# Kernel tuning notes

Measured on AMD Instinct MI355X. Metric: run time of the kernel, lower is better.

Reference implementation:

```python
import jax, jax.numpy as jnp
import numpy as np

B, K, N, D, H, DD, NB, SEQ = 1, 512, 16384, 512, 64, 64, 10, 2048
COREF_PROP = 1  # config['coref_prop']
BIG = 1e23      # additive mask penalty from the torch code


def bucket_distance(d):
    # Lee et al. style log buckets: 0,1,2,3,4, [5-7], [8-15], [16-31], [32-63], [64+]
    d = jnp.abs(d)
    logb = jnp.floor(jnp.log2(jnp.maximum(d, 1).astype(jnp.float32))).astype(d.dtype) + 3
    return jnp.clip(jnp.where(d < 5, d, logb), 0, NB - 1)


def setup_inputs() -> dict:
    key = jax.random.key(0)
    ks = jax.random.split(key, 20)
    rng = np.random.default_rng(0)
    s = 0.02
    span_begin = jnp.sort(jax.random.randint(ks[2], (B, K), 0, SEQ), axis=-1)
    return dict(
        all_span_vecs=jax.random.normal(ks[0], (B, N, D), jnp.float32),
        span_vecs=jax.random.normal(ks[1], (B, K, D), jnp.float32),
        span_begin=span_begin,
        span_end=span_begin + jax.random.randint(ks[3], (B, K), 1, 10),
        triangular_mask=jnp.broadcast_to(jnp.tril(jnp.ones((K, K), jnp.float32), -1), (B, K, K)),
        span_scores=jax.random.normal(ks[4], (B, K, 1), jnp.float32),
        prune_indices=jnp.asarray(np.sort(np.stack([rng.choice(N, K, replace=False) for _ in range(B)]), axis=-1), jnp.int32),
        span_lengths=jnp.full((B,), K, jnp.int32),
        sequence_lengths=jnp.full((B,), SEQ, jnp.int32),
        Wl=jax.random.normal(ks[5], (D, H)) * s, bl=jnp.zeros((H,), jnp.float32),
        Wr=jax.random.normal(ks[6], (D, H)) * s, br=jnp.zeros((H,), jnp.float32),
        Wp=jax.random.normal(ks[7], (D, H)) * s,
        dist_emb=jax.random.normal(ks[8], (NB, DD)) * s,
        Wd=jax.random.normal(ks[9], (DD, H)) * s, bd=jnp.zeros((H,), jnp.float32),
        Wo=jax.random.normal(ks[10], (H, 1)) * s, bo=jnp.zeros((1,), jnp.float32),
        Wg1=jax.random.normal(ks[11], (2 * D, D)) * s, bg1=jnp.zeros((D,), jnp.float32),
        Wg2=jax.random.normal(ks[12], (2 * D, D)) * s, bg2=jnp.zeros((D,), jnp.float32),
        Wpr=jax.random.normal(ks[13], (D, 1)) * s, bpr=jnp.zeros((1,), jnp.float32),
    )


def reference(all_span_vecs, span_vecs, span_begin, span_end, triangular_mask,
              span_scores, prune_indices, span_lengths, sequence_lengths,
              Wl, bl, Wr, br, Wp, dist_emb, Wd, bd, Wo, bo,
              Wg1, bg1, Wg2, bg2, Wpr, bpr):
    # ----- OptFFpairs pairwise scorer: relu(left_i + right_j + prod(v_i*v_j) + dist_ij) -> scalar
    dist_idx = bucket_distance(span_begin[:, :, None] - span_begin[:, None, :])  # [B,K,K]
    dist_feat = dist_emb[dist_idx] @ Wd + bd                                     # [B,K,K,H]

    def pair_scores(u):
        left = u @ Wl + bl                                  # [B,K,H]
        right = u @ Wr + br                                 # [B,K,H]
        prod = jnp.einsum('bid,bjd,dh->bijh', u, u, Wp)     # avoids [B,K,K,D] intermediate
        h = jax.nn.relu(left[:, :, None, :] + right[:, None, :, :] + prod + dist_feat)
        return (h @ Wo + bo)[..., 0]                        # [B,K,K], i.e. squeeze(-1)

    eye = jnp.eye(K, dtype=span_vecs.dtype)[None]

    def add_scores(cs, ss):  # coref_add_scores: add span scores as rows+cols, zero diagonal
        cs = cs + ss + jnp.swapaxes(ss, -1, -2)
        return cs * (1.0 - eye)

    def gate(Wg, bg, left, right):  # MyGate: g = sigmoid(W[l;r]); g*l + (1-g)*r
        g = jax.nn.sigmoid(jnp.concatenate([left, right], -1) @ Wg + bg)
        return g * left + (1.0 - g) * right

    update = span_vecs
    cs = add_scores(pair_scores(update), span_scores)
    m1 = (1.0 - triangular_mask) * BIG
    m2 = (1.0 - jnp.swapaxes(triangular_mask, 1, 2)) * BIG
    for _ in range(COREF_PROP):
        p1 = jax.nn.softmax(cs - m1, axis=-1)
        p2 = jax.nn.softmax(cs - m2, axis=-1)
        c1 = p1 @ update
        c2 = p2 @ update
        update = gate(Wg1, bg1, update, c1) + gate(Wg2, bg2, update, c2)
        # update_coref_scores=True: rescore with pruner(update)
        cs = add_scores(pair_scores(update), update @ Wpr + bpr)

    # ----- overwrite_spans: masked scatter of updated filtered spans into all spans
    mask = (jnp.arange(K)[None, :] < span_lengths[:, None])[..., None]  # [B,K,1]
    b_idx = jnp.arange(B)[:, None]
    orig = all_span_vecs[b_idx, prune_indices]                          # [B,K,D]
    all_out = all_span_vecs.at[b_idx, prune_indices].set(jnp.where(mask, update, orig))
    return all_out, update, cs
```

## Files before the change

### kernel.cpp

```cpp
#include <hip/hip_runtime.h>
#include <hip/hip_bf16.h>


typedef __bf16 bf16;
typedef bf16 bf16x8 __attribute__((ext_vector_type(8)));
typedef float f32x4 __attribute__((ext_vector_type(4)));
typedef float f32x16 __attribute__((ext_vector_type(16)));

#define MFMA16(a, b, c) __builtin_amdgcn_mfma_f32_16x16x32_bf16((a), (b), (c), 0, 0, 0)
#define MFMA32(a, b, c) __builtin_amdgcn_mfma_f32_32x32x16_bf16((a), (b), (c), 0, 0, 0)

__device__ __forceinline__ void gll16(const bf16* g, bf16* lds) {
  __builtin_amdgcn_global_load_lds(
      (const __attribute__((address_space(1))) unsigned int*)g,
      (__attribute__((address_space(3))) unsigned int*)lds, 16, 0, 0);
}

__global__ void k_prep(const float* __restrict__ sv,
                       const float* __restrict__ Wl, const float* __restrict__ Wr,
                       const float* __restrict__ Wg1, const float* __restrict__ Wg2,
                       const float* __restrict__ de, const float* __restrict__ Wd,
                       const float* __restrict__ bd, const float* __restrict__ bl,
                       const float* __restrict__ br, const float* __restrict__ bg1,
                       const float* __restrict__ bg2, const float* __restrict__ Wp,
                       bf16* __restrict__ u1, bf16* __restrict__ ugb,
                       bf16* __restrict__ wlr, float* __restrict__ blbr,
                       float* __restrict__ bgc, bf16* __restrict__ wgb,
                       float* __restrict__ dtab, bf16* __restrict__ wpTb)
{
  const int total = 262144 + 65536 + 128 + 1048576 + 1024 + 640 + 32768;
  for (int idx0 = blockIdx.x * 256 + threadIdx.x; idx0 < total; idx0 += 2048 * 256) {
    int k = idx0;
    if (k < 262144) {
      float v = sv[k]; bf16 b = (bf16)v; u1[k] = b;
      int i = k >> 9, d = k & 511;
      ugb[(long)i * 1024 + d] = b;
      ugb[524288 + (long)i * 1024 + d] = b;
      continue;
    }
    k -= 262144;
    if (k < 65536) {
      int d = k >> 7, h = k & 127;
      wlr[k] = (bf16)(h < 64 ? Wl[d * 64 + h] : Wr[d * 64 + h - 64]);
      continue;
    }
    k -= 65536;
    if (k < 128) { blbr[k] = (k < 64 ? bl[k] : br[k - 64]); continue; }
    k -= 128;
    if (k < 1048576) {
      wgb[k] = (bf16)(k < 524288 ? Wg1[k] : Wg2[k - 524288]);
      continue;
    }
    k -= 1048576;
    if (k < 1024) { bgc[k] = (k < 512 ? bg1[k] : bg2[k - 512]); continue; }
    k -= 1024;
    if (k < 640) {
      int b_ = k >> 6, h = k & 63;
      float s = bd[h];
      for (int e = 0; e < 64; ++e) s += de[b_ * 64 + e] * Wd[e * 64 + h];
      dtab[k] = s;
      continue;
    }
    k -= 640;
    {
      int h = k >> 9, d = k & 511;
      wpTb[k] = (bf16)Wp[d * 64 + h];
    }
  }
}

__global__ __launch_bounds__(256, 2) void k_gemm(
    const bf16* __restrict__ A, int lda, long asz,
    const bf16* __restrict__ B, int ldb, long bsz,
    float* __restrict__ C, int ldc, long csz,
    const float* __restrict__ bias, int bstride, int K,
    bf16* __restrict__ xout)
{
  __shared__ bf16 As[64 * 40];
  __shared__ bf16 Bs[64 * 40];
  const int t = threadIdx.x, lane = t & 63, wave = t >> 6;
  const int tc = blockIdx.x, tr = blockIdx.y, z = blockIdx.z;
  A += (long)z * asz; B += (long)z * bsz; C += (long)z * csz;
  const int wr = wave >> 1, wc = wave & 1;
  const int arow = t >> 2, aslot = t & 3;
  const int s = lane >> 4, rr = lane & 15;
  f32x4 acc00 = {}, acc01 = {}, acc10 = {}, acc11 = {};
  const int nk = K >> 5;
  for (int kk = 0; kk < nk; ++kk) {
    __syncthreads();
    *(uint4*)&As[arow * 40 + aslot * 8] =
        *(const uint4*)(A + (long)(tr * 64 + arow) * lda + kk * 32 + aslot * 8);
    {
      const bf16* bsrc = B + (long)(kk * 32 + aslot * 8) * ldb + tc * 64 + arow;
      bf16x8 tv;
#pragma unroll
      for (int e = 0; e < 8; ++e) tv[e] = bsrc[(long)e * ldb];
      *(bf16x8*)&Bs[arow * 40 + aslot * 8] = tv;
    }
    __syncthreads();
    bf16x8 a0 = *(const bf16x8*)&As[(wr * 32 + rr) * 40 + s * 8];
    bf16x8 a1 = *(const bf16x8*)&As[(wr * 32 + 16 + rr) * 40 + s * 8];
    bf16x8 b0 = *(const bf16x8*)&Bs[(wc * 32 + rr) * 40 + s * 8];
    bf16x8 b1 = *(const bf16x8*)&Bs[(wc * 32 + 16 + rr) * 40 + s * 8];
    acc00 = MFMA16(a0, b0, acc00);
    acc01 = MFMA16(a0, b1, acc01);
    acc10 = MFMA16(a1, b0, acc10);
    acc11 = MFMA16(a1, b1, acc11);
  }
#pragma unroll
  for (int mf = 0; mf < 2; ++mf) {
#pragma unroll
    for (int nf = 0; nf < 2; ++nf) {
      f32x4 v = mf == 0 ? (nf == 0 ? acc00 : acc01) : (nf == 0 ? acc10 : acc11);
      int col = tc * 64 + wc * 32 + nf * 16 + rr;
      float bi = bias ? bias[z * bstride + col] : 0.f;
      int row0 = tr * 64 + wr * 32 + mf * 16 + s * 4;
#pragma unroll
      for (int r = 0; r < 4; ++r) {
        float val = v[r] + bi;
        int row = row0 + r;
        C[(long)row * ldc + col] = val;
        if (xout) {
          long gidx = (row < 512)
              ? ((long)row * 1024 + 512 + col)
              : (524288 + (long)(row - 512) * 1024 + 512 + col);
          xout[gidx] = (bf16)val;
        }
      }
    }
  }
}

__global__ __launch_bounds__(512, 1) void k_pair64(
    const bf16* __restrict__ Ubf, const float* __restrict__ Uf,
    const bf16* __restrict__ wpTb, const float* __restrict__ LR,
    const float* __restrict__ dtabg, const int* __restrict__ sb,
    const float* __restrict__ ss, const float* __restrict__ Wo,
    const float* __restrict__ bo, float* __restrict__ cs,
    const float* __restrict__ copysrc, float* __restrict__ copydst, int docopy)
{
  __shared__ bf16 Apan[2][256 * 64];
  __shared__ bf16 Bpan[2][256 * 64];
  __shared__ float dtsp[10 * 68];
  __shared__ int sbt[256];

  const int t = threadIdx.x;
  const int l = t & 63;
  const int w = t >> 6;
  const int wm = w >> 1, wn = w & 1;
  const int hi = l >> 5, l31 = l & 31;
  const int jb = blockIdx.x;
  const int mt = blockIdx.y;
  const int i0 = mt * 4;
  const int i = i0 + wm;

  for (int idx = t; idx < 640; idx += 512)
    dtsp[(idx >> 6) * 68 + (idx & 63)] = dtabg[idx];
  if (t < 256) sbt[t] = sb[jb * 256 + t];

  const bf16* bsrcq[4];
  bf16* bdstq[4];
#pragma unroll
  for (int q = 0; q < 4; ++q) {
    int u = q * 512 + t;
    int r = u >> 3, c = u & 7;
    bsrcq[q] = Ubf + (long)(jb * 256 + r) * 512 + ((c ^ (r & 7)) * 8);
    bdstq[q] = &Bpan[0][0] + q * 4096 + w * 512;
  }
  const float* uapq[4];
  const bf16* wppq[4];
  int awbq[4];
#pragma unroll
  for (int q = 0; q < 4; ++q) {
    int u = q * 512 + t;
    int m = u >> 3, c = u & 7;
    int koff = (c ^ (m & 7)) * 8;
    uapq[q] = Uf + (long)(i0 + (m >> 6)) * 512 + koff;
    wppq[q] = wpTb + (long)(m & 63) * 512 + koff;
    awbq[q] = m * 128 + c * 16;
  }

  int aoff[2][4], boff[4][4];
#pragma unroll
  for (int rf = 0; rf < 2; ++rf)
#pragma unroll
    for (int ks = 0; ks < 4; ++ks) {
      int r = wm * 64 + rf * 32 + l31;
      aoff[rf][ks] = r * 128 + (((ks * 2 + hi) ^ (r & 7)) * 16);
    }
#pragma unroll
  for (int cf = 0; cf < 4; ++cf)
#pragma unroll
    for (int ks = 0; ks < 4; ++ks) {
      int r = wn * 128 + cf * 32 + l31;
      boff[cf][ks] = r * 128 + (((ks * 2 + hi) ^ (r & 7)) * 16);
    }

  {
#pragma unroll
    for (int q = 0; q < 4; ++q) gll16(bsrcq[q], bdstq[q]);
#pragma unroll
    for (int q = 0; q < 4; ++q) {
      float4 f0 = *(const float4*)uapq[q];
      float4 f1 = *(const float4*)(uapq[q] + 4);
      bf16x8 wv = *(const bf16x8*)wppq[q];
      bf16x8 v;
#pragma unroll
      for (int e = 0; e < 4; ++e) {
        v[e] = (bf16)(f0[e] * (float)wv[e]);
        v[e + 4] = (bf16)(f1[e] * (float)wv[e + 4]);
      }
      *(bf16x8*)((char*)&Apan[0][0] + awbq[q]) = v;
    }
  }
  asm volatile("s_waitcnt vmcnt(0)");
  __syncthreads();

  f32x16 acc[2][4] = {};

  for (int kc = 0; kc < 8; ++kc) {
    const int cur = kc & 1;
    float4 nf0[4], nf1[4];
    bf16x8 nwv[4];
    if (kc < 7) {
#pragma unroll
      for (int q = 0; q < 4; ++q)
        gll16(bsrcq[q] + (kc + 1) * 64, bdstq[q] + (cur ^ 1) * 16384);
#pragma unroll
      for (int q = 0; q < 4; ++q) {
        nf0[q] = *(const float4*)(uapq[q] + (kc + 1) * 64);
        nf1[q] = *(const float4*)(uapq[q] + (kc + 1) * 64 + 4);
        nwv[q] = *(const bf16x8*)(wppq[q] + (kc + 1) * 64);
      }
    }
    const char* Ab = (const char*)&Apan[cur][0];
    const char* Bb = (const char*)&Bpan[cur][0];
#pragma unroll
    for (int ks = 0; ks < 4; ++ks) {
      bf16x8 af0 = *(const bf16x8*)(Ab + aoff[0][ks]);
      bf16x8 af1 = *(const bf16x8*)(Ab + aoff[1][ks]);
      bf16x8 bf0 = *(const bf16x8*)(Bb + boff[0][ks]);
      bf16x8 bf1 = *(const bf16x8*)(Bb + boff[1][ks]);
      bf16x8 bf2 = *(const bf16x8*)(Bb + boff[2][ks]);
      bf16x8 bf3 = *(const bf16x8*)(Bb + boff[3][ks]);
      __builtin_amdgcn_s_setprio(1);
      acc[0][0] = MFMA32(af0, bf0, acc[0][0]);
      acc[0][1] = MFMA32(af0, bf1, acc[0][1]);
      acc[0][2] = MFMA32(af0, bf2, acc[0][2]);
      acc[0][3] = MFMA32(af0, bf3, acc[0][3]);
      acc[1][0] = MFMA32(af1, bf0, acc[1][0]);
      acc[1][1] = MFMA32(af1, bf1, acc[1][1]);
      acc[1][2] = MFMA32(af1, bf2, acc[1][2]);
      acc[1][3] = MFMA32(af1, bf3, acc[1][3]);
      __builtin_amdgcn_s_setprio(0);
    }
    if (kc < 7) {
      asm volatile("s_waitcnt vmcnt(0)");
      char* Ad = (char*)&Apan[cur ^ 1][0];
#pragma unroll
      for (int q = 0; q < 4; ++q) {
        bf16x8 v;
#pragma unroll
        for (int e = 0; e < 4; ++e) {
          v[e] = (bf16)(nf0[q][e] * (float)nwv[q][e]);
          v[e + 4] = (bf16)(nf1[q][e] * (float)nwv[q][e + 4]);
        }
        *(bf16x8*)(Ad + awbq[q]) = v;
      }
    }
    __syncthreads();
  }

  float4 wo_t[2][4], lf_t[2][4];
#pragma unroll
  for (int rf = 0; rf < 2; ++rf)
#pragma unroll
    for (int g = 0; g < 4; ++g) {
      wo_t[rf][g] = *(const float4*)&Wo[rf * 32 + 4 * hi + 8 * g];
      lf_t[rf][g] = *(const float4*)&LR[i * 128 + rf * 32 + 4 * hi + 8 * g];
    }
  const float ssi = ss[i];
  const int sbi = sb[i];
  const float bo0 = bo[0];
#pragma unroll
  for (int cf = 0; cf < 4; ++cf) {
    int jl = wn * 128 + cf * 32 + l31;
    int j = jb * 256 + jl;
    int dd = sbi - sbt[jl];
    int ad = dd < 0 ? -dd : dd;
    int bkt = ad < 5 ? ad : (31 - __clz(ad)) + 3;
    bkt = bkt > 9 ? 9 : bkt;
    float ssj = ss[j];
    float sum = 0.f;
#pragma unroll
    for (int rf = 0; rf < 2; ++rf) {
#pragma unroll
      for (int g = 0; g < 4; ++g) {
        float4 dt4 = *(const float4*)&dtsp[bkt * 68 + rf * 32 + 4 * hi + 8 * g];
        float4 rt4 = *(const float4*)&LR[j * 128 + 64 + rf * 32 + 4 * hi + 8 * g];
#pragma unroll
        for (int e = 0; e < 4; ++e) {
          float v = acc[rf][cf][g * 4 + e] + lf_t[rf][g][e] + rt4[e] + dt4[e];
          v = fmaxf(v, 0.f);
          sum += v * wo_t[rf][g][e];
        }
      }
    }
    sum += __shfl_xor(sum, 32);
    float val = (j == i) ? 0.f : (sum + bo0 + ssi + ssj);
    if (hi == 0) cs[(long)i * 512 + j] = val;
  }

  if (docopy) {
    const float4* s4 = (const float4*)copysrc;
    float4* d4 = (float4*)copydst;
    int idx = (mt * 2 + jb) * 512 + t;
#pragma unroll
    for (int q = 0; q < 16; ++q)
      d4[(long)q * 131072 + idx] = s4[(long)q * 131072 + idx];
  }
}

#define P2_BUILD(DST, A00, A01, A10, A11, W0, W1)                \
  {                                                              \
    bf16x8 v0, v1;                                               \
    _Pragma("unroll") for (int e = 0; e < 4; ++e) {              \
      v0[e] = (bf16)((A00)[e] * (float)(W0)[e]);                 \
      v0[e + 4] = (bf16)((A01)[e] * (float)(W0)[e + 4]);         \
      v1[e] = (bf16)((A10)[e] * (float)(W1)[e]);                 \
      v1[e + 4] = (bf16)((A11)[e] * (float)(W1)[e + 4]);         \
    }                                                            \
    *(bf16x8*)((DST) + awb0) = v0;                               \
    *(bf16x8*)((DST) + awb1) = v1;                               \
  }

#define P2_ITER(KC, bA00, bA01, bA10, bA11, bW0, bW1, rA00, rA01, rA10, rA11, rW0, rW1) \
  {                                                                                     \
    const int bcur = (KC) % 3, bnxt = ((KC) + 1) % 3, bpre = ((KC) + 2) % 3;            \
    asm volatile("s_waitcnt lgkmcnt(0)");                                               \
    asm volatile("s_waitcnt vmcnt(14)");                                                \
    __builtin_amdgcn_sched_barrier(0);                                                  \
    __builtin_amdgcn_s_barrier();                                                       \
    const char* Ab = Abase + bcur * 16384;                                              \
    const char* Bb = Bbase + bcur * 16384;                                              \
    _Pragma("unroll") for (int ks = 0; ks < 2; ++ks) {                                  \
      bf16x8 af0 = *(const bf16x8*)(Ab + aoff[0][ks]);                                  \
      bf16x8 af1 = *(const bf16x8*)(Ab + aoff[1][ks]);                                  \
      bf16x8 bf0 = *(const bf16x8*)(Bb + boff[0][ks]);                                  \
      bf16x8 bf1 = *(const bf16x8*)(Bb + boff[1][ks]);                                  \
      bf16x8 bf2 = *(const bf16x8*)(Bb + boff[2][ks]);                                  \
      bf16x8 bf3 = *(const bf16x8*)(Bb + boff[3][ks]);                                  \
      __builtin_amdgcn_s_setprio(1);                                                    \
      acc[0][0] = MFMA32(af0, bf0, acc[0][0]);                                          \
      acc[0][1] = MFMA32(af0, bf1, acc[0][1]);                                          \
      acc[0][2] = MFMA32(af0, bf2, acc[0][2]);                                          \
      acc[0][3] = MFMA32(af0, bf3, acc[0][3]);                                          \
      acc[1][0] = MFMA32(af1, bf0, acc[1][0]);                                          \
      acc[1][1] = MFMA32(af1, bf1, acc[1][1]);                                          \
      acc[1][2] = MFMA32(af1, bf2, acc[1][2]);                                          \
      acc[1][3] = MFMA32(af1, bf3, acc[1][3]);                                          \
      __builtin_amdgcn_s_setprio(0);                                                    \
    }                                                                                   \
    if ((KC) < 15) { P2_BUILD(Abase + bnxt * 16384, bA00, bA01, bA10, bA11, bW0, bW1) } \
    if ((KC) < 14) {                                                                    \
      bf16* Bd = (bf16*)(Bbase + bpre * 16384);                                         \
      gll16(bsrc0 + ((KC) + 2) * 32, Bd + w * 512);                                     \
      gll16(bsrc1 + ((KC) + 2) * 32, Bd + 4096 + w * 512);                              \
      rA00 = *(const float4*)(ua0p + ((KC) + 2) * 32);                                  \
      rA01 = *(const float4*)(ua0p + ((KC) + 2) * 32 + 4);                              \
      rA10 = *(const float4*)(ua1p + ((KC) + 2) * 32);                                  \
      rA11 = *(const float4*)(ua1p + ((KC) + 2) * 32 + 4);                              \
      rW0 = *(const bf16x8*)(wp0p + ((KC) + 2) * 32);                                   \
      rW1 = *(const bf16x8*)(wp1p + ((KC) + 2) * 32);                                   \
    }                                                                                   \
  }

__global__ __launch_bounds__(512, 1) void k_pair2(
    const bf16* __restrict__ Ubf, const float* __restrict__ Uf,
    const bf16* __restrict__ wpTb, const float* __restrict__ LR,
    const float* __restrict__ dtabg, const int* __restrict__ sb,
    const float* __restrict__ ss, const float* __restrict__ Wo,
    const float* __restrict__ bo, float* __restrict__ cs)
{
  __shared__ bf16 Apan[3][256 * 32];
  __shared__ bf16 Bpan[3][256 * 32];
  __shared__ float dtsp[10 * 68];
  __shared__ int sbt[256];

  const int t = threadIdx.x;
  const int l = t & 63;
  const int w = t >> 6;
  const int wm = w >> 1, wn = w & 1;
  const int hi = l >> 5, l31 = l & 31;
  const int jb = blockIdx.x;
  const int mt = blockIdx.y;
  const int i0 = mt * 4;
  const int i = i0 + wm;

  for (int idx = t; idx < 640; idx += 512)
    dtsp[(idx >> 6) * 68 + (idx & 63)] = dtabg[idx];
  if (t < 256) sbt[t] = sb[jb * 256 + t];

  const bf16 *bsrc0, *bsrc1;
  {
    int r0 = t >> 2, c0 = t & 3;
    int r1 = 128 + (t >> 2);
    bsrc0 = Ubf + (long)(jb * 256 + r0) * 512 + ((c0 ^ ((r0 >> 1) & 3)) * 8);
    bsrc1 = Ubf + (long)(jb * 256 + r1) * 512 + ((c0 ^ ((r1 >> 1) & 3)) * 8);
  }
  const int ar0 = t >> 2, ar1 = 128 + (t >> 2), as0 = t & 3;
  const int awb0 = ar0 * 64 + ((as0 ^ ((ar0 >> 1) & 3)) * 16);
  const int awb1 = ar1 * 64 + ((as0 ^ ((ar1 >> 1) & 3)) * 16);
  const float* ua0p = Uf + (long)(i0 + (ar0 >> 6)) * 512 + as0 * 8;
  const float* ua1p = Uf + (long)(i0 + (ar1 >> 6)) * 512 + as0 * 8;
  const bf16* wp0p = wpTb + (long)(ar0 & 63) * 512 + as0 * 8;
  const bf16* wp1p = wpTb + (long)(ar1 & 63) * 512 + as0 * 8;

  int aoff[2][2], boff[4][2];
#pragma unroll
  for (int rf = 0; rf < 2; ++rf)
#pragma unroll
    for (int ks = 0; ks < 2; ++ks) {
      int r = wm * 64 + rf * 32 + l31;
      aoff[rf][ks] = r * 64 + (((ks * 2 + hi) ^ ((r >> 1) & 3)) * 16);
    }
#pragma unroll
  for (int cf = 0; cf < 4; ++cf)
#pragma unroll
    for (int ks = 0; ks < 2; ++ks) {
      int r = wn * 128 + cf * 32 + l31;
      boff[cf][ks] = r * 64 + (((ks * 2 + hi) ^ ((r >> 1) & 3)) * 16);
    }

  char* Abase = (char*)&Apan[0][0];
  char* Bbase = (char*)&Bpan[0][0];

  float4 aA00, aA01, aA10, aA11; bf16x8 wA0, wA1;
  float4 aB00, aB01, aB10, aB11; bf16x8 wB0, wB1;
  gll16(bsrc0, (bf16*)Bbase + w * 512);
  gll16(bsrc1, (bf16*)Bbase + 4096 + w * 512);
  aA00 = *(const float4*)ua0p;        aA01 = *(const float4*)(ua0p + 4);
  aA10 = *(const float4*)ua1p;        aA11 = *(const float4*)(ua1p + 4);
  wA0 = *(const bf16x8*)wp0p;         wA1 = *(const bf16x8*)wp1p;
  gll16(bsrc0 + 32, (bf16*)(Bbase + 16384) + w * 512);
  gll16(bsrc1 + 32, (bf16*)(Bbase + 16384) + 4096 + w * 512);
  aB00 = *(const float4*)(ua0p + 32); aB01 = *(const float4*)(ua0p + 36);
  aB10 = *(const float4*)(ua1p + 32); aB11 = *(const float4*)(ua1p + 36);
  wB0 = *(const bf16x8*)(wp0p + 32);  wB1 = *(const bf16x8*)(wp1p + 32);
  P2_BUILD(Abase, aA00, aA01, aA10, aA11, wA0, wA1)

  f32x16 acc[2][4] = {};

  for (int kq = 0; kq < 8; ++kq) {
    const int kc = kq * 2;
    P2_ITER(kc, aB00, aB01, aB10, aB11, wB0, wB1,
            aA00, aA01, aA10, aA11, wA0, wA1)
    P2_ITER(kc + 1, aA00, aA01, aA10, aA11, wA0, wA1,
            aB00, aB01, aB10, aB11, wB0, wB1)
  }

  float4 wo_t[2][4], lf_t[2][4];
#pragma unroll
  for (int rf = 0; rf < 2; ++rf)
#pragma unroll
    for (int g = 0; g < 4; ++g) {
      wo_t[rf][g] = *(const float4*)&Wo[rf * 32 + 4 * hi + 8 * g];
      lf_t[rf][g] = *(const float4*)&LR[i * 128 + rf * 32 + 4 * hi + 8 * g];
    }
  const float ssi = ss[i];
  const int sbi = sb[i];
  const float bo0 = bo[0];
#pragma unroll
  for (int cf = 0; cf < 4; ++cf) {
    int jl = wn * 128 + cf * 32 + l31;
    int j = jb * 256 + jl;
    int dd = sbi - sbt[jl];
    int ad = dd < 0 ? -dd : dd;
    int bkt = ad < 5 ? ad : (31 - __clz(ad)) + 3;
    bkt = bkt > 9 ? 9 : bkt;
    float ssj = ss[j];
    float sum = 0.f;
#pragma unroll
    for (int rf = 0; rf < 2; ++rf) {
#pragma unroll
      for (int g = 0; g < 4; ++g) {
        float4 dt4 = *(const float4*)&dtsp[bkt * 68 + rf * 32 + 4 * hi + 8 * g];
        float4 rt4 = *(const float4*)&LR[j * 128 + 64 + rf * 32 + 4 * hi + 8 * g];
#pragma unroll
        for (int e = 0; e < 4; ++e) {
          float v = acc[rf][cf][g * 4 + e] + lf_t[rf][g][e] + rt4[e] + dt4[e];
          v = fmaxf(v, 0.f);
          sum += v * wo_t[rf][g][e];
        }
      }
    }
    sum += __shfl_xor(sum, 32);
    float val = (j == i) ? 0.f : (sum + bo0 + ssi + ssj);
    if (hi == 0) cs[(long)i * 512 + j] = val;
  }
}

__global__ __launch_bounds__(64) void k_softmax(const float* __restrict__ cs,
                                                bf16* __restrict__ p12)
{
  int b = blockIdx.x, kind = b >> 9, i = b & 511, lane = threadIdx.x;
  const float* row = cs + i * 512;
  float v[8];
  float4 x0 = *(const float4*)(row + lane * 8);
  float4 x1 = *(const float4*)(row + lane * 8 + 4);
  v[0] = x0.x; v[1] = x0.y; v[2] = x0.z; v[3] = x0.w;
  v[4] = x1.x; v[5] = x1.y; v[6] = x1.z; v[7] = x1.w;
  bool any = (kind == 0) ? (i > 0) : (i < 511);
  bf16x8 ov;
  if (!any) {
    float u = 1.0f / 512.0f;
#pragma unroll
    for (int e = 0; e < 8; ++e) ov[e] = (bf16)u;
  } else {
    float m = -3.4e38f;
#pragma unroll
    for (int e = 0; e < 8; ++e) {
      int jj = lane * 8 + e;
      bool valid = (kind == 0) ? (jj < i) : (jj > i);
      if (valid) m = fmaxf(m, v[e]);
    }
    m = fmaxf(m, __shfl_xor(m, 1));  m = fmaxf(m, __shfl_xor(m, 2));
    m = fmaxf(m, __shfl_xor(m, 4));  m = fmaxf(m, __shfl_xor(m, 8));
    m = fmaxf(m, __shfl_xor(m, 16)); m = fmaxf(m, __shfl_xor(m, 32));
    float p[8]; float ssum = 0.f;
#pragma unroll
    for (int e = 0; e < 8; ++e) {
      int jj = lane * 8 + e;
      bool valid = (kind == 0) ? (jj < i) : (jj > i);
      p[e] = valid ? __expf(v[e] - m) : 0.f;
      ssum += p[e];
    }
    ssum += __shfl_xor(ssum, 1);  ssum += __shfl_xor(ssum, 2);
    ssum += __shfl_xor(ssum, 4);  ssum += __shfl_xor(ssum, 8);
    ssum += __shfl_xor(ssum, 16); ssum += __shfl_xor(ssum, 32);
    float inv = 1.0f / ssum;
#pragma unroll
    for (int e = 0; e < 8; ++e) ov[e] = (bf16)(p[e] * inv);
  }
  *(bf16x8*)(p12 + (long)b * 512 + lane * 8) = ov;
}

__global__ __launch_bounds__(512) void k_mid2(
    const float* __restrict__ sv, const float* __restrict__ c12,
    const float* __restrict__ G12, const float* __restrict__ Wpr,
    const float* __restrict__ bpr, const bf16* __restrict__ wlr,
    const float* __restrict__ blbr, const int* __restrict__ pi,
    const int* __restrict__ sl, float* __restrict__ upd,
    bf16* __restrict__ u2, float* __restrict__ ss2,
    float* __restrict__ lr2, float* __restrict__ out_all)
{
  __shared__ float upl[512];
  __shared__ float red[8];
  __shared__ float part2[4][128];
  const int i = blockIdx.x;
  const int t = threadIdx.x;
  const long ii = (long)i * 512 + t;

  float u = sv[ii], c1 = c12[ii], c2 = c12[262144 + ii];
  float g1 = 1.f / (1.f + __expf(-G12[ii]));
  float g2 = 1.f / (1.f + __expf(-G12[262144 + ii]));
  float up = g1 * u + (1.f - g1) * c1 + g2 * u + (1.f - g2) * c2;
  upd[ii] = up;
  u2[ii] = (bf16)up;
  upl[t] = up;
  if (i < sl[0]) out_all[(long)pi[i] * 512 + t] = up;

  float pd = up * Wpr[t];
  pd += __shfl_xor(pd, 1);  pd += __shfl_xor(pd, 2);  pd += __shfl_xor(pd, 4);
  pd += __shfl_xor(pd, 8);  pd += __shfl_xor(pd, 16); pd += __shfl_xor(pd, 32);
  if ((t & 63) == 0) red[t >> 6] = pd;
  __syncthreads();
  if (t == 0) {
    float s = 0.f;
#pragma unroll
    for (int e = 0; e < 8; ++e) s += red[e];
    ss2[i] = s + bpr[0];
  }

  const int n = t & 127, part = t >> 7;
  float s = 0.f;
  const int d0 = part * 128;
#pragma unroll 4
  for (int d2 = 0; d2 < 128; ++d2)
    s += upl[d0 + d2] * (float)wlr[(d0 + d2) * 128 + n];
  part2[part][n] = s;
  __syncthreads();
  if (t < 128)
    lr2[(long)i * 128 + t] =
        part2[0][t] + part2[1][t] + part2[2][t] + part2[3][t] + blbr[t];
}

extern "C" void kernel_launch(void* const* d_in, const int* in_sizes, int n_in,
                              void* d_out, int out_size, void* d_ws, size_t ws_size,
                              hipStream_t stream)
{
  const float* asv = (const float*)d_in[0];
  const float* sv = (const float*)d_in[1];
  const int* sb = (const int*)d_in[2];
  const float* sscore = (const float*)d_in[5];
  const int* pi = (const int*)d_in[6];
  const int* sl = (const int*)d_in[7];
  const float* Wl = (const float*)d_in[9];
  const float* bl = (const float*)d_in[10];
  const float* Wr = (const float*)d_in[11];
  const float* br = (const float*)d_in[12];
  const float* Wp = (const float*)d_in[13];
  const float* de = (const float*)d_in[14];
  const float* Wd = (const float*)d_in[15];
  const float* bd = (const float*)d_in[16];
  const float* Wo = (const float*)d_in[17];
  const float* bo = (const float*)d_in[18];
  const float* Wg1 = (const float*)d_in[19];
  const float* bg1 = (const float*)d_in[20];
  const float* Wg2 = (const float*)d_in[21];
  const float* bg2 = (const float*)d_in[22];
  const float* Wpr = (const float*)d_in[23];
  const float* bpr = (const float*)d_in[24];

  float* out_all = (float*)d_out;
  float* out_upd = out_all + 8388608;
  float* out_cs = out_all + 8650752;

  char* w = (char*)d_ws;
  size_t off = 0;
  auto take = [&](size_t bytes) -> void* {
    void* p = w + off;
    off = (off + bytes + 255) & ~(size_t)255;
    return p;
  };
  bf16* u1b = (bf16*)take(524288);
  bf16* u2b = (bf16*)take(524288);
  bf16* wlr = (bf16*)take(131072);
  bf16* wgb = (bf16*)take(2097152);
  float* blbr = (float*)take(512);
  float* bgc = (float*)take(4096);
  float* dtab = (float*)take(2560);
  bf16* wpTb = (bf16*)take(65536);
  float* lr1 = (float*)take(262144);
  float* lr2 = (float*)take(262144);
  float* cs1 = (float*)take(1048576);
  bf16* p12 = (bf16*)take(1048576);
  float* c12 = (float*)take(4194304);
  bf16* ugb = (bf16*)take(2097152);
  float* G12 = (float*)take(2097152);
  float* ss2 = (float*)take(2048);

  k_prep<<<2048, 256, 0, stream>>>(sv, Wl, Wr, Wg1, Wg2, de, Wd, bd, bl, br, bg1, bg2,
                                   Wp, u1b, ugb, wlr, blbr, bgc, wgb, dtab, wpTb);
  k_gemm<<<dim3(2, 8, 1), 256, 0, stream>>>(u1b, 512, 0, wlr, 128, 0, lr1, 128, 0,
                                            blbr, 0, 512, nullptr);
  k_pair64<<<dim3(2, 128), 512, 0, stream>>>(u1b, sv, wpTb, lr1, dtab, sb, sscore, Wo,
                                             bo, cs1, asv, out_all, 1);
  k_softmax<<<1024, 64, 0, stream>>>(cs1, p12);
  k_gemm<<<dim3(8, 16, 1), 256, 0, stream>>>(p12, 512, 0, u1b, 512, 0, c12, 512, 0,
                                             nullptr, 0, 512, ugb);
  k_gemm<<<dim3(8, 8, 2), 256, 0, stream>>>(ugb, 1024, 524288, wgb, 512, 524288,
                                            G12, 512, 262144, bgc, 512, 1024, nullptr);
  k_mid2<<<512, 512, 0, stream>>>(sv, c12, G12, Wpr, bpr, wlr, blbr, pi, sl,
                                  out_upd, u2b, ss2, lr2, out_all);
  k_pair2<<<dim3(2, 128), 512, 0, stream>>>(u2b, out_upd, wpTb, lr2, dtab, sb, ss2,
                                            Wo, bo, out_cs);
}
```

Measured before the change: 144.4 us.

## Split gate GEMM and fold update-half into the first projection GEMM

The gate input [u;c]@Wg is split into u@Wg_top + c@Wg_bot. The u@Wg_top part is computed once, together with the Wl/Wr projection, as one wider GEMM (N=1152) on the initial update. The gate GEMM then only runs over the c half with K=512 and adds the precomputed term in its epilogue. This halves the K dimension of the batched gate GEMM and removes the concatenated ugb buffer writes, at the cost of a wider first GEMM and an extra strided read in the epilogue.

```diff
diff --git a/kernel.cpp b/kernel.cpp
--- a/kernel.cpp
+++ b/kernel.cpp
@@ -23,37 +23,44 @@
                        const float* __restrict__ bd, const float* __restrict__ bl,
                        const float* __restrict__ br, const float* __restrict__ bg1,
                        const float* __restrict__ bg2, const float* __restrict__ Wp,
-                       bf16* __restrict__ u1, bf16* __restrict__ ugb,
-                       bf16* __restrict__ wlr, float* __restrict__ blbr,
-                       float* __restrict__ bgc, bf16* __restrict__ wgb,
+                       bf16* __restrict__ u1, bf16* __restrict__ wext,
+                       float* __restrict__ bext, bf16* __restrict__ wgbot,
                        float* __restrict__ dtab, bf16* __restrict__ wpTb)
 {
-  const int total = 262144 + 65536 + 128 + 1048576 + 1024 + 640 + 32768;
+  const int total = 262144 + 589824 + 1152 + 524288 + 640 + 32768;
   for (int idx0 = blockIdx.x * 256 + threadIdx.x; idx0 < total; idx0 += 2048 * 256) {
     int k = idx0;
     if (k < 262144) {
-      float v = sv[k]; bf16 b = (bf16)v; u1[k] = b;
-      int i = k >> 9, d = k & 511;
-      ugb[(long)i * 1024 + d] = b;
-      ugb[524288 + (long)i * 1024 + d] = b;
+      u1[k] = (bf16)sv[k];
       continue;
     }
     k -= 262144;
-    if (k < 65536) {
-      int d = k >> 7, h = k & 127;
-      wlr[k] = (bf16)(h < 64 ? Wl[d * 64 + h] : Wr[d * 64 + h - 64]);
+    if (k < 589824) {
+      int d = k / 1152, n = k % 1152;
+      float v;
+      if (n < 64) v = Wl[d * 64 + n];
+      else if (n < 128) v = Wr[d * 64 + n - 64];
+      else if (n < 640) v = Wg1[d * 512 + (n - 128)];
+      else v = Wg2[d * 512 + (n - 640)];
+      wext[k] = (bf16)v;
       continue;
     }
-    k -= 65536;
-    if (k < 128) { blbr[k] = (k < 64 ? bl[k] : br[k - 64]); continue; }
-    k -= 128;
-    if (k < 1048576) {
-      wgb[k] = (bf16)(k < 524288 ? Wg1[k] : Wg2[k - 524288]);
+    k -= 589824;
+    if (k < 1152) {
+      float v;
+      if (k < 64) v = bl[k];
+      else if (k < 128) v = br[k - 64];
+      else if (k < 640) v = bg1[k - 128];
+      else v = bg2[k - 640];
+      bext[k] = v;
       continue;
     }
-    k -= 1048576;
-    if (k < 1024) { bgc[k] = (k < 512 ? bg1[k] : bg2[k - 512]); continue; }
-    k -= 1024;
+    k -= 1152;
+    if (k < 524288) {
+      wgbot[k] = (bf16)((k < 262144) ? Wg1[262144 + k] : Wg2[k]);
+      continue;
+    }
+    k -= 524288;
     if (k < 640) {
       int b_ = k >> 6, h = k & 63;
       float s = bd[h];
@@ -73,7 +80,8 @@
     const bf16* __restrict__ A, int lda, long asz,
     const bf16* __restrict__ B, int ldb, long bsz,
     float* __restrict__ C, int ldc, long csz,
-    const float* __restrict__ bias, int bstride, int K,
+    const float* __restrict__ bias, int K,
+    const float* __restrict__ addm, long addm_zs, int addm_ld,
     bf16* __restrict__ xout)
 {
   __shared__ bf16 As[64 * 40];
@@ -113,19 +121,15 @@
     for (int nf = 0; nf < 2; ++nf) {
       f32x4 v = mf == 0 ? (nf == 0 ? acc00 : acc01) : (nf == 0 ? acc10 : acc11);
       int col = tc * 64 + wc * 32 + nf * 16 + rr;
-      float bi = bias ? bias[z * bstride + col] : 0.f;
+      float bi = bias ? bias[col] : 0.f;
       int row0 = tr * 64 + wr * 32 + mf * 16 + s * 4;
 #pragma unroll
       for (int r = 0; r < 4; ++r) {
+        int row = row0 + r;
         float val = v[r] + bi;
-        int row = row0 + r;
+        if (addm) val += addm[z * addm_zs + (long)row * addm_ld + col];
         C[(long)row * ldc + col] = val;
-        if (xout) {
-          long gidx = (row < 512)
-              ? ((long)row * 1024 + 512 + col)
-              : (524288 + (long)(row - 512) * 1024 + 512 + col);
-          xout[gidx] = (bf16)val;
-        }
+        if (xout) xout[(long)row * 512 + col] = (bf16)val;
       }
     }
   }
@@ -133,7 +137,7 @@
 
 __global__ __launch_bounds__(512, 1) void k_pair64(
     const bf16* __restrict__ Ubf, const float* __restrict__ Uf,
-    const bf16* __restrict__ wpTb, const float* __restrict__ LR,
+    const bf16* __restrict__ wpTb, const float* __restrict__ LR, int ldlr,
     const float* __restrict__ dtabg, const int* __restrict__ sb,
     const float* __restrict__ ss, const float* __restrict__ Wo,
     const float* __restrict__ bo, float* __restrict__ cs,
@@ -277,7 +281,7 @@
 #pragma unroll
     for (int g = 0; g < 4; ++g) {
       wo_t[rf][g] = *(const float4*)&Wo[rf * 32 + 4 * hi + 8 * g];
-      lf_t[rf][g] = *(const float4*)&LR[i * 128 + rf * 32 + 4 * hi + 8 * g];
+      lf_t[rf][g] = *(const float4*)&LR[(long)i * ldlr + rf * 32 + 4 * hi + 8 * g];
     }
   const float ssi = ss[i];
   const int sbi = sb[i];
@@ -297,7 +301,7 @@
 #pragma unroll
       for (int g = 0; g < 4; ++g) {
         float4 dt4 = *(const float4*)&dtsp[bkt * 68 + rf * 32 + 4 * hi + 8 * g];
-        float4 rt4 = *(const float4*)&LR[j * 128 + 64 + rf * 32 + 4 * hi + 8 * g];
+        float4 rt4 = *(const float4*)&LR[(long)j * ldlr + 64 + rf * 32 + 4 * hi + 8 * g];
 #pragma unroll
         for (int e = 0; e < 4; ++e) {
           float v = acc[rf][cf][g * 4 + e] + lf_t[rf][g][e] + rt4[e] + dt4[e];
@@ -377,7 +381,7 @@
 
 __global__ __launch_bounds__(512, 1) void k_pair2(
     const bf16* __restrict__ Ubf, const float* __restrict__ Uf,
-    const bf16* __restrict__ wpTb, const float* __restrict__ LR,
+    const bf16* __restrict__ wpTb, const float* __restrict__ LR, int ldlr,
     const float* __restrict__ dtabg, const int* __restrict__ sb,
     const float* __restrict__ ss, const float* __restrict__ Wo,
     const float* __restrict__ bo, float* __restrict__ cs)
@@ -465,7 +469,7 @@
 #pragma unroll
     for (int g = 0; g < 4; ++g) {
       wo_t[rf][g] = *(const float4*)&Wo[rf * 32 + 4 * hi + 8 * g];
-      lf_t[rf][g] = *(const float4*)&LR[i * 128 + rf * 32 + 4 * hi + 8 * g];
+      lf_t[rf][g] = *(const float4*)&LR[(long)i * ldlr + rf * 32 + 4 * hi + 8 * g];
     }
   const float ssi = ss[i];
   const int sbi = sb[i];
@@ -485,7 +489,7 @@
 #pragma unroll
       for (int g = 0; g < 4; ++g) {
         float4 dt4 = *(const float4*)&dtsp[bkt * 68 + rf * 32 + 4 * hi + 8 * g];
-        float4 rt4 = *(const float4*)&LR[j * 128 + 64 + rf * 32 + 4 * hi + 8 * g];
+        float4 rt4 = *(const float4*)&LR[(long)j * ldlr + 64 + rf * 32 + 4 * hi + 8 * g];
 #pragma unroll
         for (int e = 0; e < 4; ++e) {
           float v = acc[rf][cf][g * 4 + e] + lf_t[rf][g][e] + rt4[e] + dt4[e];
@@ -548,8 +552,8 @@
 __global__ __launch_bounds__(512) void k_mid2(
     const float* __restrict__ sv, const float* __restrict__ c12,
     const float* __restrict__ G12, const float* __restrict__ Wpr,
-    const float* __restrict__ bpr, const bf16* __restrict__ wlr,
-    const float* __restrict__ blbr, const int* __restrict__ pi,
+    const float* __restrict__ bpr, const bf16* __restrict__ wext, int ldw,
+    const float* __restrict__ bext, const int* __restrict__ pi,
     const int* __restrict__ sl, float* __restrict__ upd,
     bf16* __restrict__ u2, float* __restrict__ ss2,
     float* __restrict__ lr2, float* __restrict__ out_all)
@@ -587,12 +591,12 @@
   const int d0 = part * 128;
 #pragma unroll 4
   for (int d2 = 0; d2 < 128; ++d2)
-    s += upl[d0 + d2] * (float)wlr[(d0 + d2) * 128 + n];
+    s += upl[d0 + d2] * (float)wext[(long)(d0 + d2) * ldw + n];
   part2[part][n] = s;
   __syncthreads();
   if (t < 128)
     lr2[(long)i * 128 + t] =
-        part2[0][t] + part2[1][t] + part2[2][t] + part2[3][t] + blbr[t];
+        part2[0][t] + part2[1][t] + part2[2][t] + part2[3][t] + bext[t];
 }
 
 extern "C" void kernel_launch(void* const* d_in, const int* in_sizes, int n_in,
@@ -635,34 +639,34 @@
   };
   bf16* u1b = (bf16*)take(524288);
   bf16* u2b = (bf16*)take(524288);
-  bf16* wlr = (bf16*)take(131072);
-  bf16* wgb = (bf16*)take(2097152);
-  float* blbr = (float*)take(512);
-  float* bgc = (float*)take(4096);
+  bf16* wext = (bf16*)take(1179648);
+  float* bext = (float*)take(4608);
+  bf16* wgbot = (bf16*)take(1048576);
   float* dtab = (float*)take(2560);
   bf16* wpTb = (bf16*)take(65536);
-  float* lr1 = (float*)take(262144);
+  float* LE = (float*)take(2359296);
   float* lr2 = (float*)take(262144);
   float* cs1 = (float*)take(1048576);
   bf16* p12 = (bf16*)take(1048576);
-  float* c12 = (float*)take(4194304);
-  bf16* ugb = (bf16*)take(2097152);
+  float* c12 = (float*)take(2097152);
+  bf16* cb = (bf16*)take(1048576);
   float* G12 = (float*)take(2097152);
   float* ss2 = (float*)take(2048);
 
   k_prep<<<2048, 256, 0, stream>>>(sv, Wl, Wr, Wg1, Wg2, de, Wd, bd, bl, br, bg1, bg2,
-                                   Wp, u1b, ugb, wlr, blbr, bgc, wgb, dtab, wpTb);
-  k_gemm<<<dim3(2, 8, 1), 256, 0, stream>>>(u1b, 512, 0, wlr, 128, 0, lr1, 128, 0,
-                                            blbr, 0, 512, nullptr);
-  k_pair64<<<dim3(2, 128), 512, 0, stream>>>(u1b, sv, wpTb, lr1, dtab, sb, sscore, Wo,
-                                             bo, cs1, asv, out_all, 1);
+                                   Wp, u1b, wext, bext, wgbot, dtab, wpTb);
+  k_gemm<<<dim3(18, 8, 1), 256, 0, stream>>>(u1b, 512, 0, wext, 1152, 0, LE, 1152, 0,
+                                             bext, 512, nullptr, 0, 0, nullptr);
+  k_pair64<<<dim3(2, 128), 512, 0, stream>>>(u1b, sv, wpTb, LE, 1152, dtab, sb,
+                                             sscore, Wo, bo, cs1, asv, out_all, 1);
   k_softmax<<<1024, 64, 0, stream>>>(cs1, p12);
   k_gemm<<<dim3(8, 16, 1), 256, 0, stream>>>(p12, 512, 0, u1b, 512, 0, c12, 512, 0,
-                                             nullptr, 0, 512, ugb);
-  k_gemm<<<dim3(8, 8, 2), 256, 0, stream>>>(ugb, 1024, 524288, wgb, 512, 524288,
-                                            G12, 512, 262144, bgc, 512, 1024, nullptr);
-  k_mid2<<<512, 512, 0, stream>>>(sv, c12, G12, Wpr, bpr, wlr, blbr, pi, sl,
+                                             nullptr, 512, nullptr, 0, 0, cb);
+  k_gemm<<<dim3(8, 8, 2), 256, 0, stream>>>(cb, 512, 262144, wgbot, 512, 262144,
+                                            G12, 512, 262144, nullptr, 512,
+                                            LE + 128, 512, 1152, nullptr);
+  k_mid2<<<512, 512, 0, stream>>>(sv, c12, G12, Wpr, bpr, wext, 1152, bext, pi, sl,
                                   out_upd, u2b, ss2, lr2, out_all);
-  k_pair2<<<dim3(2, 128), 512, 0, stream>>>(u2b, out_upd, wpTb, lr2, dtab, sb, ss2,
-                                            Wo, bo, out_cs);
-}
+  k_pair2<<<dim3(2, 128), 512, 0, stream>>>(u2b, out_upd, wpTb, lr2, 128, dtab, sb,
+                                            ss2, Wo, bo, out_cs);
+}
```

Result: faster. 137.0 us (-5.1%).
